# Optimization experiments

Hardware: AMD Instinct MI355X
Metric: run time of the kernel (lower is better)

## Reference

```python
import jax, jax.numpy as jnp
import numpy as np
import math

EMBED_DIM = 1024
NUM_HEADS = 16
HEAD_DIM = EMBED_DIM // NUM_HEADS


def alibi_slopes(num_heads: int) -> np.ndarray:
    def slopes_pow2(n):
        start = 2.0 ** (-(2.0 ** (-(math.log2(n) - 3))))
        return [start * (start ** i) for i in range(n)]
    if math.log2(num_heads).is_integer():
        return np.array(slopes_pow2(num_heads), dtype=np.float32)
    closest = 2 ** math.floor(math.log2(num_heads))
    extra = slopes_pow2(2 * closest)[closest:]
    return np.array(slopes_pow2(closest) + extra[: num_heads - closest], dtype=np.float32)


def setup_inputs() -> dict:
    key = jax.random.key(0)
    ks = jax.random.split(key, 9)
    B, S, E = 2, 2048, EMBED_DIM
    scale = 1.0 / math.sqrt(E)
    x = jax.random.normal(ks[0], (B, S, E), dtype=jnp.float32)
    Wq = jax.random.normal(ks[1], (E, E), dtype=jnp.float32) * scale
    Wk = jax.random.normal(ks[2], (E, E), dtype=jnp.float32) * scale
    Wv = jax.random.normal(ks[3], (E, E), dtype=jnp.float32) * scale
    Wo = jax.random.normal(ks[4], (E, E), dtype=jnp.float32) * scale
    bq = jax.random.normal(ks[5], (E,), dtype=jnp.float32) * 0.01
    bk = jax.random.normal(ks[6], (E,), dtype=jnp.float32) * 0.01
    bv = jax.random.normal(ks[7], (E,), dtype=jnp.float32) * 0.01
    bo = jax.random.normal(ks[8], (E,), dtype=jnp.float32) * 0.01
    return {"x": x, "Wq": Wq, "bq": bq, "Wk": Wk, "bk": bk,
            "Wv": Wv, "bv": bv, "Wo": Wo, "bo": bo}


def reference(x, Wq, bq, Wk, bk, Wv, bv, Wo, bo):
    B, S, E = x.shape
    H, D = NUM_HEADS, HEAD_DIM
    # Linear layers (torch convention: y = x @ W.T + b)
    q = (x @ Wq.T + bq).reshape(B, S, H, D).transpose(0, 2, 1, 3)  # [B,H,S,D]
    k = (x @ Wk.T + bk).reshape(B, S, H, D).transpose(0, 2, 1, 3)
    v = (x @ Wv.T + bv).reshape(B, S, H, D).transpose(0, 2, 1, 3)

    # ALiBi bias: -slope_h * |i - j|
    slopes = jnp.asarray(alibi_slopes(H))                      # [H]
    pos = jnp.arange(S, dtype=jnp.float32)
    rel = jnp.abs(pos[None, :] - pos[:, None])                 # [S,S]
    bias = -slopes[:, None, None] * rel[None, :, :]            # [H,S,S]

    scores = jnp.einsum('bhqd,bhkd->bhqk', q, k) / math.sqrt(D)
    scores = scores + bias[None]
    causal = jnp.tril(jnp.ones((S, S), dtype=bool))            # keep lower triangle
    scores = jnp.where(causal[None, None], scores, -jnp.inf)
    probs = jax.nn.softmax(scores, axis=-1)
    out = jnp.einsum('bhqk,bhkd->bhqd', probs, v)              # [B,H,S,D]
    out = out.transpose(0, 2, 1, 3).reshape(B, S, E)
    return out @ Wo.T + bo
```

## Files before the change

kernel.cpp:

```cpp
#include <hip/hip_runtime.h>
#include <hip/hip_bf16.h>

typedef __bf16 bf16;
typedef __bf16 bf16x4 __attribute__((ext_vector_type(4)));
typedef __bf16 bf16x8 __attribute__((ext_vector_type(8)));
typedef float  f32x4  __attribute__((ext_vector_type(4)));

#define NEG_BIG (-1e30f)
#define LOG2E 1.44269504088896340736f

#define AS1(p) ((const __attribute__((address_space(1))) void*)(p))
#define AS3(p) ((__attribute__((address_space(3))) void*)(p))

__device__ __forceinline__ void stage16(const void* g, void* lds_uniform_base) {
    __builtin_amdgcn_global_load_lds(AS1(g), AS3(lds_uniform_base), 16, 0, 0);
}

__device__ __forceinline__ bf16x8 cvt8(const float* __restrict__ p) {
    bf16x8 r;
#pragma unroll
    for (int i = 0; i < 8; ++i) r[i] = (bf16)p[i];
    return r;
}

template <int CTRL>
__device__ __forceinline__ float dpp_max_step(float x) {
    int v = __builtin_bit_cast(int, x);
    int s = __builtin_amdgcn_update_dpp(v, v, CTRL, 0xF, 0xF, true);
    return fmaxf(x, __builtin_bit_cast(float, s));
}
template <int CTRL>
__device__ __forceinline__ float dpp_add_step(float x) {
    int v = __builtin_bit_cast(int, x);
    int s = __builtin_amdgcn_update_dpp(v, v, CTRL, 0xF, 0xF, true);
    return x + __builtin_bit_cast(float, s);
}
__device__ __forceinline__ float red16_max(float x) {
    x = dpp_max_step<0xB1>(x);
    x = dpp_max_step<0x4E>(x);
    x = dpp_max_step<0x141>(x);
    x = dpp_max_step<0x140>(x);
    return x;
}
__device__ __forceinline__ float red16_sum(float x) {
    x = dpp_add_step<0xB1>(x);
    x = dpp_add_step<0x4E>(x);
    x = dpp_add_step<0x141>(x);
    x = dpp_add_step<0x140>(x);
    return x;
}

#if __has_builtin(__builtin_amdgcn_exp2f)
#define EXP2F(x) __builtin_amdgcn_exp2f(x)
#else
#define EXP2F(x) exp2f(x)
#endif

__global__ __launch_bounds__(256) void conv_all(
    const float* __restrict__ x,  const float* __restrict__ wq,
    const float* __restrict__ wk, const float* __restrict__ wv,
    bf16* __restrict__ xb, bf16* __restrict__ wb)
{
    const int blk = blockIdx.x;
    const float* src; bf16* dst; size_t off;
    if (blk < 2048)      { src = x;  dst = xb;           off = (size_t)blk * 2048; }
    else if (blk < 2560) { src = wq; dst = wb;           off = (size_t)(blk - 2048) * 2048; }
    else if (blk < 3072) { src = wk; dst = wb + 1048576; off = (size_t)(blk - 2560) * 2048; }
    else                 { src = wv; dst = wb + 2097152; off = (size_t)(blk - 3072) * 2048; }
    const size_t i = off + (size_t)threadIdx.x * 8;
    *(bf16x8*)(dst + i) = cvt8(src + i);
}

__global__ __launch_bounds__(256) void qkv_gemm(
    const bf16* __restrict__ Xb, const bf16* __restrict__ Wb,
    const float* __restrict__ bq, const float* __restrict__ bk, const float* __restrict__ bv,
    bf16* __restrict__ qo, bf16* __restrict__ ko, bf16* __restrict__ vo)
{
    __shared__ alignas(16) bf16 As[128 * 32];
    __shared__ alignas(16) bf16 Bs[128 * 32];

    const int t    = threadIdx.x;
    const int lane = t & 63, w = t >> 6;
    const int quad = lane >> 4, col = lane & 15;
    const int nt = blockIdx.x;
    const int mt = blockIdx.y;
    const int region = nt >> 3;
    const int n0 = (nt & 7) * 128;
    const int m0 = mt * 128;
    const int K  = 1024;

    const bf16*  W    = Wb + (size_t)region * 1048576;
    const float* bias = region == 0 ? bq : (region == 1 ? bk : bv);

    const int wm = (w >> 1) * 64, wn = (w & 1) * 64;
    f32x4 acc[4][4] = {};

    for (int k0 = 0; k0 < K; k0 += 32) {
        __syncthreads();
#pragma unroll
        for (int i = 0; i < 2; ++i) {
            int c = i * 256 + t;
            stage16(Xb + (size_t)(m0 + (c >> 2)) * K + k0 + (c & 3) * 8,
                    As + (i * 256 + w * 64) * 8);
        }
#pragma unroll
        for (int i = 0; i < 2; ++i) {
            int c = i * 256 + t;
            stage16(W + (size_t)(n0 + (c >> 2)) * K + k0 + (c & 3) * 8,
                    Bs + (i * 256 + w * 64) * 8);
        }
        __syncthreads();

        bf16x8 a[4], b[4];
#pragma unroll
        for (int i = 0; i < 4; ++i)
            a[i] = *(const bf16x8*)(As + (wm + i * 16 + col) * 32 + quad * 8);
#pragma unroll
        for (int j = 0; j < 4; ++j)
            b[j] = *(const bf16x8*)(Bs + (wn + j * 16 + col) * 32 + quad * 8);
#pragma unroll
        for (int i = 0; i < 4; ++i)
#pragma unroll
            for (int j = 0; j < 4; ++j)
                acc[i][j] = __builtin_amdgcn_mfma_f32_16x16x32_bf16(a[i], b[j], acc[i][j], 0, 0, 0);
    }

    if (region == 2) {
#pragma unroll
        for (int i = 0; i < 4; ++i) {
            const int mbase = m0 + wm + i * 16 + quad * 4;
            const int b_ = mbase >> 11, s = mbase & 2047;
#pragma unroll
            for (int j = 0; j < 4; ++j) {
                const int n = n0 + wn + j * 16 + col;
                const float bb = bias[n];
                const int h = n >> 6, d = n & 63;
                bf16x4 pk;
#pragma unroll
                for (int r = 0; r < 4; ++r) pk[r] = (bf16)(acc[i][j][r] + bb);
                *(bf16x4*)(vo + ((size_t)(b_ * 16 + h) * 64 + d) * 2048 + s) = pk;
            }
        }
    } else {
        bf16* out = region == 0 ? qo : ko;
        const float scale = region == 0 ? (0.125f * LOG2E) : 1.0f;
#pragma unroll
        for (int i = 0; i < 4; ++i) {
            const int mbase = m0 + wm + i * 16 + quad * 4;
#pragma unroll
            for (int j = 0; j < 4; ++j) {
                const int n = n0 + wn + j * 16 + col;
                const float bb = bias[n];
                const int h = n >> 6, d = n & 63;
#pragma unroll
                for (int r = 0; r < 4; ++r) {
                    const int m  = mbase + r;
                    const int b_ = m >> 11, s = m & 2047;
                    out[(((size_t)(b_ * 16 + h)) * 2048 + s) * 64 + d] =
                        (bf16)((acc[i][j][r] + bb) * scale);
                }
            }
        }
    }
}

__global__ __launch_bounds__(512) void attn_kernel(
    const bf16* __restrict__ Q, const bf16* __restrict__ Kg,
    const bf16* __restrict__ Vt, bf16* __restrict__ O)
{
    const int t    = threadIdx.x;
    const int lane = t & 63, w = t >> 6;
    const int quad = lane >> 4, col = lane & 15;
    const int bh   = blockIdx.x & 31;
    const int pair = blockIdx.x >> 5;
    const int b  = bh >> 4, h = bh & 15;
    const float nslope = -EXP2F(-0.5f * (float)(h + 1)) * LOG2E;

    const bf16* qp  = Q  + (size_t)bh * 2048 * 64;
    const bf16* kp  = Kg + (size_t)bh * 2048 * 64;
    const bf16* vtp = Vt + (size_t)bh * 64 * 2048;

    __shared__ alignas(16) bf16 Kbuf[2][128 * 64];
    __shared__ alignas(16) bf16 Vbuf[2][64 * 128];
    __shared__ alignas(16) bf16 Ps[8 * 16 * 136];
    bf16* Pw = Ps + w * (16 * 136);

    for (int pass = 0; pass < 2; ++pass) {
        const int qt = pass == 0 ? (15 - pair) : pair;
        const int q0 = qt * 128;

        bf16x8 qa[2];
#pragma unroll
        for (int ks = 0; ks < 2; ++ks)
            qa[ks] = *(const bf16x8*)(qp + (size_t)(q0 + w * 16 + col) * 64
                                      + ks * 32 + quad * 8);

        float mrow[4], lrow[4], bi[4];
        f32x4 of[4] = {};
        const int gi0 = q0 + w * 16 + quad * 4;
#pragma unroll
        for (int r = 0; r < 4; ++r) {
            mrow[r] = NEG_BIG; lrow[r] = 0.f;
            bi[r] = nslope * (float)(gi0 + r);
        }

        {
#pragma unroll
            for (int i = 0; i < 2; ++i) {
                int c = i * 512 + t;
                int row = c >> 3, j8 = (c & 7) ^ (row & 7);
                stage16(kp + (size_t)row * 64 + j8 * 8, Kbuf[0] + (i * 512 + w * 64) * 8);
            }
#pragma unroll
            for (int i = 0; i < 2; ++i) {
                int c = i * 512 + t;
                int d = c >> 4, j8 = (c & 15) ^ (d & 7);
                stage16(vtp + (size_t)d * 2048 + j8 * 8, Vbuf[0] + (i * 512 + w * 64) * 8);
            }
        }
        __syncthreads();

        for (int kvt = 0; kvt <= qt; ++kvt) {
            const int kv0 = kvt * 128;
            const bf16* Kb = Kbuf[kvt & 1];
            const bf16* Vb = Vbuf[kvt & 1];

            if (kvt < qt) {
                bf16* Kn = Kbuf[(kvt & 1) ^ 1];
                bf16* Vn = Vbuf[(kvt & 1) ^ 1];
                const int nv0 = kv0 + 128;
#pragma unroll
                for (int i = 0; i < 2; ++i) {
                    int c = i * 512 + t;
                    int row = c >> 3, j8 = (c & 7) ^ (row & 7);
                    stage16(kp + (size_t)(nv0 + row) * 64 + j8 * 8, Kn + (i * 512 + w * 64) * 8);
                }
#pragma unroll
                for (int i = 0; i < 2; ++i) {
                    int c = i * 512 + t;
                    int d = c >> 4, j8 = (c & 15) ^ (d & 7);
                    stage16(vtp + (size_t)d * 2048 + nv0 + j8 * 8, Vn + (i * 512 + w * 64) * 8);
                }
            }

            f32x4 sc[8];
#pragma unroll
            for (int nj = 0; nj < 8; ++nj) {
                const int row = nj * 16 + col;
                const bf16* kb = Kb + row * 64;
                const int rx = row & 7;
                bf16x8 k0f = *(const bf16x8*)(kb + (quad ^ rx) * 8);
                bf16x8 k1f = *(const bf16x8*)(kb + ((quad + 4) ^ rx) * 8);
                f32x4 z = {};
                z = __builtin_amdgcn_mfma_f32_16x16x32_bf16(qa[0], k0f, z, 0, 0, 0);
                z = __builtin_amdgcn_mfma_f32_16x16x32_bf16(qa[1], k1f, z, 0, 0, 0);
                sc[nj] = z;
            }

            const bool diag = (kvt == qt);
            float bj[8];
#pragma unroll
            for (int nj = 0; nj < 8; ++nj)
                bj[nj] = nslope * (float)(kv0 + nj * 16 + col);

#pragma unroll
            for (int r = 0; r < 4; ++r) {
#pragma unroll
                for (int nj = 0; nj < 8; ++nj)
                    sc[nj][r] += bi[r] - bj[nj];
                if (diag) {
                    const int gi = gi0 + r;
#pragma unroll
                    for (int nj = 0; nj < 8; ++nj)
                        if (kv0 + nj * 16 + col > gi) sc[nj][r] = NEG_BIG;
                }
                float mx = sc[0][r];
#pragma unroll
                for (int nj = 1; nj < 8; ++nj) mx = fmaxf(mx, sc[nj][r]);
                mx = red16_max(mx);
                const float mo = mrow[r];
                const float mn = fmaxf(mo, mx);
                const float alpha = EXP2F(mo - mn);
                float rs = 0.f;
#pragma unroll
                for (int nj = 0; nj < 8; ++nj) {
                    float p = EXP2F(sc[nj][r] - mn);
                    sc[nj][r] = p;
                    rs += p;
                }
                rs = red16_sum(rs);
                mrow[r] = mn;
                lrow[r] = lrow[r] * alpha + rs;
#pragma unroll
                for (int jd = 0; jd < 4; ++jd) of[jd][r] *= alpha;
            }

#pragma unroll
            for (int nj = 0; nj < 8; ++nj)
#pragma unroll
                for (int r = 0; r < 4; ++r)
                    Pw[(quad * 4 + r) * 136 + nj * 16 + col] = (bf16)sc[nj][r];

#pragma unroll
            for (int kk = 0; kk < 4; ++kk) {
                bf16x8 pa = *(const bf16x8*)(Pw + col * 136 + kk * 32 + quad * 8);
#pragma unroll
                for (int jd = 0; jd < 4; ++jd) {
                    const int rd = jd * 16 + col;
                    bf16x8 vbf = *(const bf16x8*)(Vb + rd * 128 + (((kk * 4 + quad) ^ (rd & 7)) * 8));
                    of[jd] = __builtin_amdgcn_mfma_f32_16x16x32_bf16(pa, vbf, of[jd], 0, 0, 0);
                }
            }

            __syncthreads();
        }

#pragma unroll
        for (int r = 0; r < 4; ++r) {
            const int s = q0 + w * 16 + quad * 4 + r;
            const float inv_l = 1.f / lrow[r];
#pragma unroll
            for (int jd = 0; jd < 4; ++jd) {
                const int e = h * 64 + jd * 16 + col;
                O[((size_t)(b * 2048 + s)) * 1024 + e] = (bf16)(of[jd][r] * inv_l);
            }
        }
    }
}

__global__ __launch_bounds__(256) void out_gemm(
    const bf16* __restrict__ A, const float* __restrict__ W,
    const float* __restrict__ bias, float* __restrict__ out)
{
    __shared__ alignas(16) bf16 As[128 * 32];
    __shared__ alignas(16) bf16 Bs[128 * 32];

    const int t    = threadIdx.x;
    const int lane = t & 63, w = t >> 6;
    const int quad = lane >> 4, col = lane & 15;
    const int n0 = blockIdx.x * 128;
    const int m0 = blockIdx.y * 128;
    const int K  = 1024;
    const int wm = (w >> 1) * 64, wn = (w & 1) * 64;
    const int r0 = t >> 2, c8 = (t & 3) * 8;
    f32x4 acc[4][4] = {};

    for (int k0 = 0; k0 < K; k0 += 32) {
        bf16x8 bx0 = cvt8(W + (size_t)(n0 + r0)      * K + k0 + c8);
        bf16x8 bx1 = cvt8(W + (size_t)(n0 + 64 + r0) * K + k0 + c8);
        __syncthreads();
#pragma unroll
        for (int i = 0; i < 2; ++i) {
            int c = i * 256 + t;
            stage16(A + (size_t)(m0 + (c >> 2)) * K + k0 + (c & 3) * 8,
                    As + (i * 256 + w * 64) * 8);
        }
        *(bf16x8*)(Bs + r0 * 32 + c8)        = bx0;
        *(bf16x8*)(Bs + (64 + r0) * 32 + c8) = bx1;
        __syncthreads();

        bf16x8 a[4], b[4];
#pragma unroll
        for (int i = 0; i < 4; ++i)
            a[i] = *(const bf16x8*)(As + (wm + i * 16 + col) * 32 + quad * 8);
#pragma unroll
        for (int j = 0; j < 4; ++j)
            b[j] = *(const bf16x8*)(Bs + (wn + j * 16 + col) * 32 + quad * 8);
#pragma unroll
        for (int i = 0; i < 4; ++i)
#pragma unroll
            for (int j = 0; j < 4; ++j)
                acc[i][j] = __builtin_amdgcn_mfma_f32_16x16x32_bf16(a[i], b[j], acc[i][j], 0, 0, 0);
    }

#pragma unroll
    for (int i = 0; i < 4; ++i) {
        const int mbase = m0 + wm + i * 16 + quad * 4;
#pragma unroll
        for (int j = 0; j < 4; ++j) {
            const int n = n0 + wn + j * 16 + col;
            const float bb = bias[n];
#pragma unroll
            for (int r = 0; r < 4; ++r)
                out[(size_t)(mbase + r) * 1024 + n] = acc[i][j][r] + bb;
        }
    }
}

extern "C" void kernel_launch(void* const* d_in, const int* in_sizes, int n_in,
                              void* d_out, int out_size, void* d_ws, size_t ws_size,
                              hipStream_t stream) {
    const float* x  = (const float*)d_in[0];
    const float* Wq = (const float*)d_in[1];
    const float* bq = (const float*)d_in[2];
    const float* Wk = (const float*)d_in[3];
    const float* bk = (const float*)d_in[4];
    const float* Wv = (const float*)d_in[5];
    const float* bv = (const float*)d_in[6];
    const float* Wo = (const float*)d_in[7];
    const float* bo = (const float*)d_in[8];
    float* out = (float*)d_out;

    bf16* xb  = (bf16*)d_ws;
    bf16* qws = xb  + 4194304;
    bf16* kws = qws + 4194304;
    bf16* vws = kws + 4194304;
    bf16* aws = xb;

    bf16* wb = (bf16*)d_out;

    conv_all<<<dim3(3584), 256, 0, stream>>>(x, Wq, Wk, Wv, xb, wb);
    qkv_gemm<<<dim3(24, 32), 256, 0, stream>>>(xb, wb, bq, bk, bv, qws, kws, vws);
    attn_kernel<<<dim3(256), 512, 0, stream>>>(qws, kws, vws, aws);
    out_gemm<<<dim3(8, 32), 256, 0, stream>>>(aws, Wo, bo, out);
}
```

Baseline: 210.7 us.

## Read K/V tiles directly from global memory instead of LDS double buffering

Removes the shared-memory double-buffered K and V staging and per-tile block barriers in the attention kernel, so each wave loads its MFMA operands straight from global memory. It also sets a launch-bounds minimum of two blocks per CU, now that LDS usage is much smaller. The aim is to cut LDS footprint and synchronization cost. In exchange, every wave re-fetches the same K/V data through the cache hierarchy, multiplying global/L2 traffic and exposing load latency.

```diff
diff --git a/kernel.cpp b/kernel.cpp
--- a/kernel.cpp
+++ b/kernel.cpp
@@ -164,7 +164,7 @@
     }
 }
 
-__global__ __launch_bounds__(512) void attn_kernel(
+__global__ __launch_bounds__(512, 2) void attn_kernel(
     const bf16* __restrict__ Q, const bf16* __restrict__ Kg,
     const bf16* __restrict__ Vt, bf16* __restrict__ O)
 {
@@ -180,8 +180,6 @@
     const bf16* kp  = Kg + (size_t)bh * 2048 * 64;
     const bf16* vtp = Vt + (size_t)bh * 64 * 2048;
 
-    __shared__ alignas(16) bf16 Kbuf[2][128 * 64];
-    __shared__ alignas(16) bf16 Vbuf[2][64 * 128];
     __shared__ alignas(16) bf16 Ps[8 * 16 * 136];
     bf16* Pw = Ps + w * (16 * 136);
 
@@ -204,53 +202,15 @@
             bi[r] = nslope * (float)(gi0 + r);
         }
 
-        {
-#pragma unroll
-            for (int i = 0; i < 2; ++i) {
-                int c = i * 512 + t;
-                int row = c >> 3, j8 = (c & 7) ^ (row & 7);
-                stage16(kp + (size_t)row * 64 + j8 * 8, Kbuf[0] + (i * 512 + w * 64) * 8);
-            }
-#pragma unroll
-            for (int i = 0; i < 2; ++i) {
-                int c = i * 512 + t;
-                int d = c >> 4, j8 = (c & 15) ^ (d & 7);
-                stage16(vtp + (size_t)d * 2048 + j8 * 8, Vbuf[0] + (i * 512 + w * 64) * 8);
-            }
-        }
-        __syncthreads();
-
         for (int kvt = 0; kvt <= qt; ++kvt) {
             const int kv0 = kvt * 128;
-            const bf16* Kb = Kbuf[kvt & 1];
-            const bf16* Vb = Vbuf[kvt & 1];
-
-            if (kvt < qt) {
-                bf16* Kn = Kbuf[(kvt & 1) ^ 1];
-                bf16* Vn = Vbuf[(kvt & 1) ^ 1];
-                const int nv0 = kv0 + 128;
-#pragma unroll
-                for (int i = 0; i < 2; ++i) {
-                    int c = i * 512 + t;
-                    int row = c >> 3, j8 = (c & 7) ^ (row & 7);
-                    stage16(kp + (size_t)(nv0 + row) * 64 + j8 * 8, Kn + (i * 512 + w * 64) * 8);
-                }
-#pragma unroll
-                for (int i = 0; i < 2; ++i) {
-                    int c = i * 512 + t;
-                    int d = c >> 4, j8 = (c & 15) ^ (d & 7);
-                    stage16(vtp + (size_t)d * 2048 + nv0 + j8 * 8, Vn + (i * 512 + w * 64) * 8);
-                }
-            }
 
             f32x4 sc[8];
 #pragma unroll
             for (int nj = 0; nj < 8; ++nj) {
-                const int row = nj * 16 + col;
-                const bf16* kb = Kb + row * 64;
-                const int rx = row & 7;
-                bf16x8 k0f = *(const bf16x8*)(kb + (quad ^ rx) * 8);
-                bf16x8 k1f = *(const bf16x8*)(kb + ((quad + 4) ^ rx) * 8);
+                const bf16* kb = kp + (size_t)(kv0 + nj * 16 + col) * 64;
+                bf16x8 k0f = *(const bf16x8*)(kb + quad * 8);
+                bf16x8 k1f = *(const bf16x8*)(kb + 32 + quad * 8);
                 f32x4 z = {};
                 z = __builtin_amdgcn_mfma_f32_16x16x32_bf16(qa[0], k0f, z, 0, 0, 0);
                 z = __builtin_amdgcn_mfma_f32_16x16x32_bf16(qa[1], k1f, z, 0, 0, 0);
@@ -307,12 +267,10 @@
 #pragma unroll
                 for (int jd = 0; jd < 4; ++jd) {
                     const int rd = jd * 16 + col;
-                    bf16x8 vbf = *(const bf16x8*)(Vb + rd * 128 + (((kk * 4 + quad) ^ (rd & 7)) * 8));
+                    bf16x8 vbf = *(const bf16x8*)(vtp + (size_t)rd * 2048 + kv0 + kk * 32 + quad * 8);
                     of[jd] = __builtin_amdgcn_mfma_f32_16x16x32_bf16(pa, vbf, of[jd], 0, 0, 0);
                 }
             }
-
-            __syncthreads();
         }
 
 #pragma unroll
```

Result: slower. 293.8 us (+39.4%).

## Split attention KV tile across warp pairs with transposed MFMA and merge

Applied to the files above, without the earlier changes.

Each warp now handles 32 query rows and half of the 128-key tile, with a warp pair splitting the KV columns. Operands are swapped in the MFMAs so scores are laid out as keys by rows. This replaces the DPP row reductions with a ds_swizzle plus a cross-half shuffle, and allows vectorized bf16x4 P stores and output writes. Partial softmax states are merged between paired warps through LDS at the end of each pass. Launch bounds now request 2 blocks per CU, which trades register budget for occupancy and adds an extra merge synchronization.

```diff
diff --git a/kernel.cpp b/kernel.cpp
--- a/kernel.cpp
+++ b/kernel.cpp
@@ -23,31 +23,9 @@
     return r;
 }
 
-template <int CTRL>
-__device__ __forceinline__ float dpp_max_step(float x) {
-    int v = __builtin_bit_cast(int, x);
-    int s = __builtin_amdgcn_update_dpp(v, v, CTRL, 0xF, 0xF, true);
-    return fmaxf(x, __builtin_bit_cast(float, s));
-}
-template <int CTRL>
-__device__ __forceinline__ float dpp_add_step(float x) {
-    int v = __builtin_bit_cast(int, x);
-    int s = __builtin_amdgcn_update_dpp(v, v, CTRL, 0xF, 0xF, true);
-    return x + __builtin_bit_cast(float, s);
-}
-__device__ __forceinline__ float red16_max(float x) {
-    x = dpp_max_step<0xB1>(x);
-    x = dpp_max_step<0x4E>(x);
-    x = dpp_max_step<0x141>(x);
-    x = dpp_max_step<0x140>(x);
-    return x;
-}
-__device__ __forceinline__ float red16_sum(float x) {
-    x = dpp_add_step<0xB1>(x);
-    x = dpp_add_step<0x4E>(x);
-    x = dpp_add_step<0x141>(x);
-    x = dpp_add_step<0x140>(x);
-    return x;
+__device__ __forceinline__ float swz_x16(float x) {
+    return __builtin_bit_cast(float,
+        __builtin_amdgcn_ds_swizzle(__builtin_bit_cast(int, x), 0x401F));
 }
 
 #if __has_builtin(__builtin_amdgcn_exp2f)
@@ -164,7 +142,7 @@
     }
 }
 
-__global__ __launch_bounds__(512) void attn_kernel(
+__global__ __launch_bounds__(512, 2) void attn_kernel(
     const bf16* __restrict__ Q, const bf16* __restrict__ Kg,
     const bf16* __restrict__ Vt, bf16* __restrict__ O)
 {
@@ -176,32 +154,40 @@
     const int b  = bh >> 4, h = bh & 15;
     const float nslope = -EXP2F(-0.5f * (float)(h + 1)) * LOG2E;
 
+    const int qs  = (w >> 1) * 32;
+    const int kvh = (w & 1) * 64;
+    const int qo  = w & 1;
+
     const bf16* qp  = Q  + (size_t)bh * 2048 * 64;
     const bf16* kp  = Kg + (size_t)bh * 2048 * 64;
     const bf16* vtp = Vt + (size_t)bh * 64 * 2048;
 
     __shared__ alignas(16) bf16 Kbuf[2][128 * 64];
     __shared__ alignas(16) bf16 Vbuf[2][64 * 128];
-    __shared__ alignas(16) bf16 Ps[8 * 16 * 136];
-    bf16* Pw = Ps + w * (16 * 136);
+    __shared__ alignas(16) bf16 Ps[8 * 32 * 72];
+    bf16* Pw = Ps + w * (32 * 72);
+    float* mergebuf = (float*)&Kbuf[0][0];
 
     for (int pass = 0; pass < 2; ++pass) {
         const int qt = pass == 0 ? (15 - pair) : pair;
         const int q0 = qt * 128;
 
-        bf16x8 qa[2];
-#pragma unroll
-        for (int ks = 0; ks < 2; ++ks)
-            qa[ks] = *(const bf16x8*)(qp + (size_t)(q0 + w * 16 + col) * 64
-                                      + ks * 32 + quad * 8);
-
-        float mrow[4], lrow[4], bi[4];
-        f32x4 of[4] = {};
-        const int gi0 = q0 + w * 16 + quad * 4;
-#pragma unroll
-        for (int r = 0; r < 4; ++r) {
-            mrow[r] = NEG_BIG; lrow[r] = 0.f;
-            bi[r] = nslope * (float)(gi0 + r);
+        bf16x8 qa[2][2];
+#pragma unroll
+        for (int qb = 0; qb < 2; ++qb)
+#pragma unroll
+            for (int kc = 0; kc < 2; ++kc)
+                qa[qb][kc] = *(const bf16x8*)(qp + (size_t)(q0 + qs + qb * 16 + col) * 64
+                                              + kc * 32 + quad * 8);
+
+        float m_[2], l_[2], bi[2];
+        int   gl[2];
+        f32x4 of[4][2] = {};
+#pragma unroll
+        for (int qb = 0; qb < 2; ++qb) {
+            m_[qb] = NEG_BIG; l_[qb] = 0.f;
+            gl[qb] = qs + qb * 16 + col;
+            bi[qb] = nslope * (float)(q0 + gl[qb]);
         }
 
         {
@@ -243,87 +229,115 @@
                 }
             }
 
-            f32x4 sc[8];
-#pragma unroll
-            for (int nj = 0; nj < 8; ++nj) {
-                const int row = nj * 16 + col;
+            f32x4 sc[4][2];
+#pragma unroll
+            for (int nj = 0; nj < 4; ++nj) {
+                const int row = kvh + nj * 16 + col;
                 const bf16* kb = Kb + row * 64;
                 const int rx = row & 7;
-                bf16x8 k0f = *(const bf16x8*)(kb + (quad ^ rx) * 8);
-                bf16x8 k1f = *(const bf16x8*)(kb + ((quad + 4) ^ rx) * 8);
-                f32x4 z = {};
-                z = __builtin_amdgcn_mfma_f32_16x16x32_bf16(qa[0], k0f, z, 0, 0, 0);
-                z = __builtin_amdgcn_mfma_f32_16x16x32_bf16(qa[1], k1f, z, 0, 0, 0);
-                sc[nj] = z;
+                bf16x8 kA0 = *(const bf16x8*)(kb + ((quad) ^ rx) * 8);
+                bf16x8 kA1 = *(const bf16x8*)(kb + ((quad + 4) ^ rx) * 8);
+#pragma unroll
+                for (int qb = 0; qb < 2; ++qb) {
+                    f32x4 z = {};
+                    z = __builtin_amdgcn_mfma_f32_16x16x32_bf16(kA0, qa[qb][0], z, 0, 0, 0);
+                    z = __builtin_amdgcn_mfma_f32_16x16x32_bf16(kA1, qa[qb][1], z, 0, 0, 0);
+                    sc[nj][qb] = z;
+                }
             }
 
             const bool diag = (kvt == qt);
-            float bj[8];
-#pragma unroll
-            for (int nj = 0; nj < 8; ++nj)
-                bj[nj] = nslope * (float)(kv0 + nj * 16 + col);
-
-#pragma unroll
-            for (int r = 0; r < 4; ++r) {
-#pragma unroll
-                for (int nj = 0; nj < 8; ++nj)
-                    sc[nj][r] += bi[r] - bj[nj];
-                if (diag) {
-                    const int gi = gi0 + r;
-#pragma unroll
-                    for (int nj = 0; nj < 8; ++nj)
-                        if (kv0 + nj * 16 + col > gi) sc[nj][r] = NEG_BIG;
-                }
-                float mx = sc[0][r];
-#pragma unroll
-                for (int nj = 1; nj < 8; ++nj) mx = fmaxf(mx, sc[nj][r]);
-                mx = red16_max(mx);
-                const float mo = mrow[r];
+            const float bj0 = nslope * (float)(kv0 + kvh + quad * 4);
+            const int   kvb = kvh + quad * 4;
+#pragma unroll
+            for (int qb = 0; qb < 2; ++qb) {
+                float mx = NEG_BIG;
+#pragma unroll
+                for (int nj = 0; nj < 4; ++nj)
+#pragma unroll
+                    for (int r = 0; r < 4; ++r) {
+                        float v = sc[nj][qb][r] + (bi[qb] - (bj0 + nslope * (float)(nj * 16 + r)));
+                        if (diag && (kvb + nj * 16 + r > gl[qb])) v = NEG_BIG;
+                        sc[nj][qb][r] = v;
+                        mx = fmaxf(mx, v);
+                    }
+                mx = fmaxf(mx, swz_x16(mx));
+                mx = fmaxf(mx, __shfl_xor(mx, 32, 64));
+                const float mo = m_[qb];
                 const float mn = fmaxf(mo, mx);
                 const float alpha = EXP2F(mo - mn);
                 float rs = 0.f;
 #pragma unroll
-                for (int nj = 0; nj < 8; ++nj) {
-                    float p = EXP2F(sc[nj][r] - mn);
-                    sc[nj][r] = p;
-                    rs += p;
-                }
-                rs = red16_sum(rs);
-                mrow[r] = mn;
-                lrow[r] = lrow[r] * alpha + rs;
-#pragma unroll
-                for (int jd = 0; jd < 4; ++jd) of[jd][r] *= alpha;
-            }
-
-#pragma unroll
-            for (int nj = 0; nj < 8; ++nj)
-#pragma unroll
-                for (int r = 0; r < 4; ++r)
-                    Pw[(quad * 4 + r) * 136 + nj * 16 + col] = (bf16)sc[nj][r];
-
-#pragma unroll
-            for (int kk = 0; kk < 4; ++kk) {
-                bf16x8 pa = *(const bf16x8*)(Pw + col * 136 + kk * 32 + quad * 8);
+                for (int nj = 0; nj < 4; ++nj)
+#pragma unroll
+                    for (int r = 0; r < 4; ++r) {
+                        float p = EXP2F(sc[nj][qb][r] - mn);
+                        sc[nj][qb][r] = p;
+                        rs += p;
+                    }
+                rs += swz_x16(rs);
+                rs += __shfl_xor(rs, 32, 64);
+                m_[qb] = mn;
+                l_[qb] = l_[qb] * alpha + rs;
+#pragma unroll
+                for (int jd = 0; jd < 4; ++jd) of[jd][qb] *= alpha;
+            }
+
+#pragma unroll
+            for (int qb = 0; qb < 2; ++qb)
+#pragma unroll
+                for (int nj = 0; nj < 4; ++nj) {
+                    bf16x4 pk;
+#pragma unroll
+                    for (int r = 0; r < 4; ++r) pk[r] = (bf16)sc[nj][qb][r];
+                    *(bf16x4*)(Pw + (qb * 16 + col) * 72 + nj * 16 + quad * 4) = pk;
+                }
+
+#pragma unroll
+            for (int kk = 0; kk < 2; ++kk) {
+                const int vc = (w & 1) * 8 + kk * 4 + quad;
+                bf16x8 pB0 = *(const bf16x8*)(Pw + (col)      * 72 + kk * 32 + quad * 8);
+                bf16x8 pB1 = *(const bf16x8*)(Pw + (16 + col) * 72 + kk * 32 + quad * 8);
 #pragma unroll
                 for (int jd = 0; jd < 4; ++jd) {
                     const int rd = jd * 16 + col;
-                    bf16x8 vbf = *(const bf16x8*)(Vb + rd * 128 + (((kk * 4 + quad) ^ (rd & 7)) * 8));
-                    of[jd] = __builtin_amdgcn_mfma_f32_16x16x32_bf16(pa, vbf, of[jd], 0, 0, 0);
+                    bf16x8 vA = *(const bf16x8*)(Vb + rd * 128 + ((vc ^ (rd & 7)) * 8));
+                    of[jd][0] = __builtin_amdgcn_mfma_f32_16x16x32_bf16(vA, pB0, of[jd][0], 0, 0, 0);
+                    of[jd][1] = __builtin_amdgcn_mfma_f32_16x16x32_bf16(vA, pB1, of[jd][1], 0, 0, 0);
                 }
             }
 
             __syncthreads();
         }
 
-#pragma unroll
-        for (int r = 0; r < 4; ++r) {
-            const int s = q0 + w * 16 + quad * 4 + r;
-            const float inv_l = 1.f / lrow[r];
+        {
+            float* mb = mergebuf + w * 1024;
+#pragma unroll
+            for (int jd = 0; jd < 4; ++jd)
+                *(f32x4*)(mb + jd * 256 + lane * 4) = of[jd][qo ^ 1];
+            float* mlw = (float*)Pw;
+            mlw[lane * 2]     = m_[qo ^ 1];
+            mlw[lane * 2 + 1] = l_[qo ^ 1];
+            __syncthreads();
+
+            const float* mbp = mergebuf + (w ^ 1) * 1024;
+            const float* mlp = (const float*)(Ps + (w ^ 1) * (32 * 72));
+            const float m1 = mlp[lane * 2], l1 = mlp[lane * 2 + 1];
+            const float m0 = m_[qo], l0 = l_[qo];
+            const float mt = fmaxf(m0, m1);
+            const float a0 = EXP2F(m0 - mt), a1 = EXP2F(m1 - mt);
+            const float inv = 1.f / (l0 * a0 + l1 * a1);
+            const int s = q0 + qs + qo * 16 + col;
 #pragma unroll
             for (int jd = 0; jd < 4; ++jd) {
-                const int e = h * 64 + jd * 16 + col;
-                O[((size_t)(b * 2048 + s)) * 1024 + e] = (bf16)(of[jd][r] * inv_l);
-            }
+                f32x4 o1 = *(const f32x4*)(mbp + jd * 256 + lane * 4);
+                bf16x4 pk;
+#pragma unroll
+                for (int r = 0; r < 4; ++r)
+                    pk[r] = (bf16)((of[jd][qo][r] * a0 + o1[r] * a1) * inv);
+                *(bf16x4*)(O + ((size_t)(b * 2048 + s)) * 1024 + h * 64 + jd * 16 + quad * 4) = pk;
+            }
+            __syncthreads();
         }
     }
 }
```

Result: no change. 210.0 us (-0.3%).
